# Optimization experiments

Measured on AMD Instinct MI355X. Metric: run time of the kernel, lower is better.

Reference implementation:

```python
import jax, jax.numpy as jnp
import numpy as np

N, E, F_IN, H, L = 1536, 49152, 27, 64, 32


def _ln(x, g, b, eps=1e-5):
    m = x.mean(-1, keepdims=True)
    v = ((x - m) ** 2).mean(-1, keepdims=True)
    return (x - m) * jax.lax.rsqrt(v + eps) * g + b


def _gatv2(x, src, dst, Wl, bl, Wr, br, att, bias, n):
    # PyG GATv2Conv, heads=1: alpha_ij = softmax_j( att . leaky_relu(Wl x_j + Wr x_i) )
    xl = x @ Wl + bl  # source transform [n,H]
    xr = x @ Wr + br  # target transform [n,H]
    e = jax.nn.leaky_relu(xl[src] + xr[dst], 0.2)  # [E',H]
    s = e @ att  # [E'] attention logits
    m = jax.ops.segment_max(s, dst, num_segments=n)
    w = jnp.exp(s - m[dst])
    denom = jax.ops.segment_sum(w, dst, num_segments=n)
    alpha = w / denom[dst]
    return jax.ops.segment_sum(alpha[:, None] * xl[src], dst, num_segments=n) + bias


def _model(x, eps_nodes, eps_graph, edge_index,
           Wl1, bl1, Wr1, br1, att1, bias1,
           Wl2, bl2, Wr2, br2, att2, bias2,
           Wnm, bnm, Wnv, bnv, Wgm, bgm, Wgv, bgv,
           Wd1, bd1, ln1_g, ln1_b, Wd2, bd2, ln2_g, ln2_b, Wd3, bd3,
           We1, be1, lne_g, lne_b, We2, be2,
           Wf1, bf1, lnf_g, lnf_b, Wf2, bf2):
    n = x.shape[0]
    loop = jnp.arange(n)
    src = jnp.concatenate([edge_index[0], loop])  # add self loops (PyG default)
    dst = jnp.concatenate([edge_index[1], loop])
    h = jax.nn.relu(_gatv2(x, src, dst, Wl1, bl1, Wr1, br1, att1, bias1, n))
    h = jax.nn.relu(_gatv2(h, src, dst, Wl2, bl2, Wr2, br2, att2, bias2, n))
    node_mu = h @ Wnm + bnm
    node_logvar = h @ Wnv + bnv
    gh = h.mean(0)
    graph_mu = gh @ Wgm + bgm
    graph_logvar = gh @ Wgv + bgv
    z = node_mu + eps_nodes * jnp.exp(0.5 * node_logvar)  # node reparam (training)
    _zg = graph_mu + eps_graph * jnp.exp(0.5 * graph_logvar)  # z_graph: computed, unused downstream as in source
    # dec_node_features MLP
    nf = _ln(jax.nn.relu(z @ Wd1 + bd1), ln1_g, ln1_b)
    nf = _ln(jax.nn.relu(nf @ Wd2 + bd2), ln2_g, ln2_b)
    nf = nf @ Wd3 + bd3  # [n, F_IN]
    # feature_refinement (node_embeddings = h is passed in forward)
    nf = _ln(jax.nn.relu(jnp.concatenate([nf, h], -1) @ Wf1 + bf1), lnf_g, lnf_b)
    node_features = nf @ Wf2 + bf2
    # edge_pred over all i<j pairs, vectorized (replaces the O(N^2) python loop)
    iu, ju = jnp.triu_indices(n, k=1)
    ei = jnp.concatenate([z[iu], z[ju]], -1)  # [P, 2L]
    eh = _ln(jax.nn.relu(ei @ We1 + be1), lne_g, lne_b)
    edge_logits = (eh @ We2 + be2)[:, 0]  # [P]
    return node_features, edge_logits, node_mu, node_logvar, graph_mu, graph_logvar


def setup_inputs() -> dict:
    key = jax.random.key(0)
    ki = iter(jax.random.split(key, 40))
    def W(fi, fo):
        return jax.random.normal(next(ki), (fi, fo), jnp.float32) / np.sqrt(fi)
    z64 = jnp.zeros((H,), jnp.float32)
    o64 = jnp.ones((H,), jnp.float32)
    zL = jnp.zeros((L,), jnp.float32)
    zF = jnp.zeros((F_IN,), jnp.float32)
    inp = {}
    inp["x"] = jax.random.normal(next(ki), (N, F_IN), jnp.float32)
    inp["edge_index"] = jax.random.randint(next(ki), (2, E), 0, N)
    inp["eps_nodes"] = jax.random.normal(next(ki), (N, L), jnp.float32)
    inp["eps_graph"] = jax.random.normal(next(ki), (L,), jnp.float32)
    inp.update(Wl1=W(F_IN, H), bl1=z64, Wr1=W(F_IN, H), br1=z64,
               att1=jax.random.normal(next(ki), (H,), jnp.float32) / np.sqrt(H), bias1=z64,
               Wl2=W(H, H), bl2=z64, Wr2=W(H, H), br2=z64,
               att2=jax.random.normal(next(ki), (H,), jnp.float32) / np.sqrt(H), bias2=z64)
    inp.update(Wnm=W(H, L), bnm=zL, Wnv=W(H, L), bnv=zL,
               Wgm=W(H, L), bgm=zL, Wgv=W(H, L), bgv=zL)
    inp.update(Wd1=W(L, H), bd1=z64, ln1_g=o64, ln1_b=z64,
               Wd2=W(H, H), bd2=z64, ln2_g=o64, ln2_b=z64,
               Wd3=W(H, F_IN), bd3=zF)
    inp.update(We1=W(2 * L, H), be1=z64, lne_g=o64, lne_b=z64,
               We2=W(H, 1), be2=jnp.zeros((1,), jnp.float32))
    inp.update(Wf1=W(F_IN + H, H), bf1=z64, lnf_g=o64, lnf_b=z64,
               Wf2=W(H, F_IN), bf2=zF)
    return inp


def reference(x, edge_index, eps_nodes, eps_graph,
              Wl1, bl1, Wr1, br1, att1, bias1,
              Wl2, bl2, Wr2, br2, att2, bias2,
              Wnm, bnm, Wnv, bnv, Wgm, bgm, Wgv, bgv,
              Wd1, bd1, ln1_g, ln1_b, Wd2, bd2, ln2_g, ln2_b, Wd3, bd3,
              We1, be1, lne_g, lne_b, We2, be2,
              Wf1, bf1, lnf_g, lnf_b, Wf2, bf2):
    return _model(x, eps_nodes, eps_graph, edge_index,
                  Wl1, bl1, Wr1, br1, att1, bias1,
                  Wl2, bl2, Wr2, br2, att2, bias2,
                  Wnm, bnm, Wnv, bnv, Wgm, bgm, Wgv, bgv,
                  Wd1, bd1, ln1_g, ln1_b, Wd2, bd2, ln2_g, ln2_b, Wd3, bd3,
                  We1, be1, lne_g, lne_b, We2, be2,
                  Wf1, bf1, lnf_g, lnf_b, Wf2, bf2)
```

## Files before the change

### kernel.cpp

```cpp
#include <hip/hip_runtime.h>

#define NN 1536
#define NE 49152
#define NM (NE + NN)
#define FIN 27
#define HD 64
#define LDIM 32
#define PP 1178880

#define EL_OFF  (NN*FIN)
#define MU_OFF  (EL_OFF + PP)
#define LV_OFF  (MU_OFF + NN*LDIM)
#define GMU_OFF (LV_OFF + NN*LDIM)
#define GLV_OFF (GMU_OFF + LDIM)

__device__ __forceinline__ float wsum(float v) {
#pragma unroll
  for (int m = 1; m < 64; m <<= 1) v += __shfl_xor(v, m, 64);
  return v;
}
__device__ __forceinline__ void wsum2(float& a, float& b) {
#pragma unroll
  for (int m = 1; m < 64; m <<= 1) {
    a += __shfl_xor(a, m, 64);
    b += __shfl_xor(b, m, 64);
  }
}
__device__ __forceinline__ float lnorm64(float x, float g, float b) {
  float s1 = x, s2 = x * x;
  wsum2(s1, s2);
  float mu = s1 * (1.0f / 64.0f);
  float var = fmaf(-mu, mu, s2 * (1.0f / 64.0f));
  return (x - mu) * rsqrtf(var + 1e-5f) * g + b;
}
__device__ __forceinline__ void cp4(float* dst, const float* __restrict__ src,
                                    int n4, int t) {
  const float4* s4 = (const float4*)src;
  float4* d4 = (float4*)dst;
  for (int e = t; e < n4; e += 256) d4[e] = s4[e];
}

__device__ __forceinline__ float gat_gather(const int* __restrict__ rowptr,
                                            const int* __restrict__ slot,
                                            const float* __restrict__ xl,
                                            float xri, float ak, int i, int k) {
  int beg = rowptr[i], end = rowptr[i + 1];
  float acc = 0.f, den = 0.f;
  for (int e0 = beg; e0 < end; e0 += 64) {
    int sidx = (e0 + k < end) ? slot[e0 + k] : 0;
    int nn = min(64, end - e0);
    int j = 0;
    for (; j + 1 < nn; j += 2) {
      int s0 = __shfl(sidx, j, 64), s1 = __shfl(sidx, j + 1, 64);
      float x0 = xl[s0 * HD + k], x1 = xl[s1 * HD + k];
      float e0v = x0 + xri, e1v = x1 + xri;
      e0v = fmaxf(e0v, 0.2f * e0v);
      e1v = fmaxf(e1v, 0.2f * e1v);
      float p0 = e0v * ak, p1 = e1v * ak;
      wsum2(p0, p1);
      float w0 = expf(p0), w1 = expf(p1);
      acc = fmaf(w0, x0, acc); den += w0;
      acc = fmaf(w1, x1, acc); den += w1;
    }
    if (j < nn) {
      int s0 = __shfl(sidx, j, 64);
      float x0 = xl[s0 * HD + k];
      float e0v = x0 + xri;
      e0v = fmaxf(e0v, 0.2f * e0v);
      float w0 = expf(wsum(e0v * ak));
      acc = fmaf(w0, x0, acc); den += w0;
    }
  }
  return acc / den;
}

__global__ __launch_bounds__(256) void gvae_xform1(
    const float* __restrict__ in,
    const float* __restrict__ Wl, const float* __restrict__ bl,
    const float* __restrict__ Wr, const float* __restrict__ br,
    float* __restrict__ xl, float* __restrict__ xr,
    const int* __restrict__ ei, int* __restrict__ cnt) {
  __shared__ __align__(16) float sWl[FIN * HD];
  __shared__ __align__(16) float sWr[FIN * HD];
  int t = threadIdx.x;
  int gid = blockIdx.x * 256 + t;
  if (gid < NE) atomicAdd(&cnt[ei[NE + gid]], 1);
  cp4(sWl, Wl, FIN * 16, t);
  cp4(sWr, Wr, FIN * 16, t);
  int i = blockIdx.x * 4 + (t >> 6);
  int k = t & 63;
  float xv = (k < FIN) ? in[i * FIN + k] : 0.f;
  float l0 = bl[k], l1 = 0.f, r0 = br[k], r1 = 0.f;
  __syncthreads();
#pragma unroll
  for (int a = 0; a < FIN; a += 2) {
    float xa = __shfl(xv, a, 64);
    l0 = fmaf(xa, sWl[a * HD + k], l0);
    r0 = fmaf(xa, sWr[a * HD + k], r0);
    if (a + 1 < FIN) {
      float xb = __shfl(xv, a + 1, 64);
      l1 = fmaf(xb, sWl[(a + 1) * HD + k], l1);
      r1 = fmaf(xb, sWr[(a + 1) * HD + k], r1);
    }
  }
  xl[i * HD + k] = l0 + l1;
  xr[i * HD + k] = r0 + r1;
}

__global__ __launch_bounds__(256) void gvae_scan(
    const int* __restrict__ cnt, int* __restrict__ rowptr,
    int* __restrict__ cursor, int* __restrict__ slot) {
  __shared__ int part[256];
  int t = threadIdx.x;
  int base = t * 6;
  int v[6];
  int s = 0;
#pragma unroll
  for (int j = 0; j < 6; j++) { v[j] = cnt[base + j] + 1; s += v[j]; }
  part[t] = s;
  __syncthreads();
  for (int off = 1; off < 256; off <<= 1) {
    int y = (t >= off) ? part[t - off] : 0;
    __syncthreads();
    part[t] += y;
    __syncthreads();
  }
  int r = part[t] - s;
#pragma unroll
  for (int j = 0; j < 6; j++) {
    int node = base + j;
    rowptr[node] = r;
    slot[r] = node;
    cursor[node] = r + 1;
    r += v[j];
  }
  if (t == 255) rowptr[NN] = r;
}

__global__ __launch_bounds__(256) void gvae_scatter(
    const int* __restrict__ ei, int* __restrict__ cursor, int* __restrict__ slot) {
  int m = blockIdx.x * 256 + threadIdx.x;
  if (m < NE) {
    int d = ei[NE + m];
    int p = atomicAdd(&cursor[d], 1);
    slot[p] = ei[m];
  }
}

__global__ __launch_bounds__(256) void gvae_gatherx(
    const int* __restrict__ rowptr, const int* __restrict__ slot,
    const float* __restrict__ xl, const float* __restrict__ xr,
    const float* __restrict__ att, const float* __restrict__ hbias,
    const float* __restrict__ Wl, const float* __restrict__ bl,
    const float* __restrict__ Wr, const float* __restrict__ br,
    float* __restrict__ xlo, float* __restrict__ xro) {
  __shared__ __align__(16) float sWl[HD * HD];
  __shared__ __align__(16) float sWr[HD * HD];
  int t = threadIdx.x;
  cp4(sWl, Wl, HD * 16, t);
  cp4(sWr, Wr, HD * 16, t);
  int i = blockIdx.x * 4 + (t >> 6);
  int k = t & 63;
  float xri = xr[i * HD + k];
  float ak = att[k];
  float hv = fmaxf(gat_gather(rowptr, slot, xl, xri, ak, i, k) + hbias[k], 0.f);
  float l0 = bl[k], l1 = 0.f, r0 = br[k], r1 = 0.f;
  __syncthreads();
#pragma unroll
  for (int a = 0; a < HD; a += 2) {
    float xa = __shfl(hv, a, 64);
    float xb = __shfl(hv, a + 1, 64);
    l0 = fmaf(xa, sWl[a * HD + k], l0);
    r0 = fmaf(xa, sWr[a * HD + k], r0);
    l1 = fmaf(xb, sWl[(a + 1) * HD + k], l1);
    r1 = fmaf(xb, sWr[(a + 1) * HD + k], r1);
  }
  xlo[i * HD + k] = l0 + l1;
  xro[i * HD + k] = r0 + r1;
}

#define oE1 0
#define oD1 4096
#define oD2 6144
#define oF1 10240
#define SWTOT 16064

__global__ __launch_bounds__(256, 2) void gvae_node(
    const int* __restrict__ rowptr, const int* __restrict__ slot,
    const float* __restrict__ xl, const float* __restrict__ xr,
    const float* __restrict__ att, const float* __restrict__ bias2,
    const float* __restrict__ eps,
    const float* __restrict__ Wnm, const float* __restrict__ bnm,
    const float* __restrict__ Wnv, const float* __restrict__ bnv,
    const float* __restrict__ We1, const float* __restrict__ be1,
    const float* __restrict__ Wd1, const float* __restrict__ bd1,
    const float* __restrict__ g1, const float* __restrict__ b1,
    const float* __restrict__ Wd2, const float* __restrict__ bd2,
    const float* __restrict__ g2, const float* __restrict__ b2,
    const float* __restrict__ Wd3, const float* __restrict__ bd3,
    const float* __restrict__ Wf1, const float* __restrict__ bf1,
    const float* __restrict__ gf, const float* __restrict__ bfv,
    const float* __restrict__ Wf2, const float* __restrict__ bf2,
    float* __restrict__ uo, float* __restrict__ vo,
    float* __restrict__ gh, float* __restrict__ out) {
  __shared__ __align__(16) float sW[SWTOT];
  __shared__ float ghred[256];
  int t = threadIdx.x;
  cp4(sW + oE1, We1, 1024, t);
  cp4(sW + oD1, Wd1, 512, t);
  cp4(sW + oD2, Wd2, 1024, t);
  cp4(sW + oF1, Wf1, 1456, t);

  int i = blockIdx.x * 4 + (t >> 6);
  int k = t & 63;
  int kk = k & 31;
  int kc = (k < FIN) ? k : (FIN - 1);

  float xri = xr[i * HD + k];
  float ak = att[k];
  float h2k = fmaxf(gat_gather(rowptr, slot, xl, xri, ak, i, k) + bias2[k], 0.f);
  ghred[t] = h2k;
  __syncthreads();
  if (t < 64) {
    float s = (ghred[t] + ghred[t + 64]) + (ghred[t + 128] + ghred[t + 192]);
    atomicAdd(&gh[t], s * (1.0f / NN));
  }

  const float* W = (k < 32) ? Wnm : Wnv;
  float c0 = (k < 32) ? bnm[kk] : bnv[kk];
  float c1 = 0.f, c2 = 0.f, c3 = 0.f;
#pragma unroll
  for (int a = 0; a < HD; a += 4) {
    c0 = fmaf(__shfl(h2k, a, 64),     W[a * LDIM + kk],       c0);
    c1 = fmaf(__shfl(h2k, a + 1, 64), W[(a + 1) * LDIM + kk], c1);
    c2 = fmaf(__shfl(h2k, a + 2, 64), W[(a + 2) * LDIM + kk], c2);
    c3 = fmaf(__shfl(h2k, a + 3, 64), W[(a + 3) * LDIM + kk], c3);
  }
  float acc = (c0 + c1) + (c2 + c3);
  if (k < 32) out[MU_OFF + i * LDIM + kk] = acc;
  else        out[LV_OFF + i * LDIM + kk] = acc;

  float lv = __shfl(acc, k + 32, 64);
  float zk = acc + eps[i * LDIM + kk] * expf(0.5f * lv);

  float u0 = be1[k], u1 = 0.f, v0 = 0.f, v1 = 0.f;
#pragma unroll
  for (int a = 0; a < LDIM; a += 2) {
    float za = __shfl(zk, a, 64);
    float zb = __shfl(zk, a + 1, 64);
    u0 = fmaf(za, sW[oE1 + a * HD + k], u0);
    u1 = fmaf(zb, sW[oE1 + (a + 1) * HD + k], u1);
    v0 = fmaf(za, sW[oE1 + (a + LDIM) * HD + k], v0);
    v1 = fmaf(zb, sW[oE1 + (a + 1 + LDIM) * HD + k], v1);
  }
  uo[i * HD + k] = u0 + u1;
  vo[i * HD + k] = v0 + v1;

  c0 = bd1[k]; c1 = 0.f; c2 = 0.f; c3 = 0.f;
#pragma unroll
  for (int a = 0; a < LDIM; a += 4) {
    c0 = fmaf(__shfl(zk, a, 64),     sW[oD1 + a * HD + k],       c0);
    c1 = fmaf(__shfl(zk, a + 1, 64), sW[oD1 + (a + 1) * HD + k], c1);
    c2 = fmaf(__shfl(zk, a + 2, 64), sW[oD1 + (a + 2) * HD + k], c2);
    c3 = fmaf(__shfl(zk, a + 3, 64), sW[oD1 + (a + 3) * HD + k], c3);
  }
  float nf1 = lnorm64(fmaxf((c0 + c1) + (c2 + c3), 0.f), g1[k], b1[k]);

  c0 = bd2[k]; c1 = 0.f; c2 = 0.f; c3 = 0.f;
#pragma unroll
  for (int a = 0; a < HD; a += 4) {
    c0 = fmaf(__shfl(nf1, a, 64),     sW[oD2 + a * HD + k],       c0);
    c1 = fmaf(__shfl(nf1, a + 1, 64), sW[oD2 + (a + 1) * HD + k], c1);
    c2 = fmaf(__shfl(nf1, a + 2, 64), sW[oD2 + (a + 2) * HD + k], c2);
    c3 = fmaf(__shfl(nf1, a + 3, 64), sW[oD2 + (a + 3) * HD + k], c3);
  }
  float nf2 = lnorm64(fmaxf((c0 + c1) + (c2 + c3), 0.f), g2[k], b2[k]);

  c0 = 0.f; c1 = 0.f; c2 = 0.f; c3 = 0.f;
#pragma unroll
  for (int a = 0; a < HD; a += 4) {
    c0 = fmaf(__shfl(nf2, a, 64),     Wd3[a * FIN + kc],       c0);
    c1 = fmaf(__shfl(nf2, a + 1, 64), Wd3[(a + 1) * FIN + kc], c1);
    c2 = fmaf(__shfl(nf2, a + 2, 64), Wd3[(a + 2) * FIN + kc], c2);
    c3 = fmaf(__shfl(nf2, a + 3, 64), Wd3[(a + 3) * FIN + kc], c3);
  }
  float nf3 = (k < FIN) ? ((c0 + c1) + (c2 + c3) + bd3[kc]) : 0.f;

  c0 = bf1[k]; c1 = 0.f; c2 = 0.f; c3 = 0.f;
#pragma unroll
  for (int j = 0; j < FIN; j++) {
    float nj = __shfl(nf3, j, 64);
    c0 = fmaf(nj, sW[oF1 + j * HD + k], c0);
  }
#pragma unroll
  for (int a = 0; a < HD; a += 4) {
    c0 = fmaf(__shfl(h2k, a, 64),     sW[oF1 + (FIN + a) * HD + k],     c0);
    c1 = fmaf(__shfl(h2k, a + 1, 64), sW[oF1 + (FIN + a + 1) * HD + k], c1);
    c2 = fmaf(__shfl(h2k, a + 2, 64), sW[oF1 + (FIN + a + 2) * HD + k], c2);
    c3 = fmaf(__shfl(h2k, a + 3, 64), sW[oF1 + (FIN + a + 3) * HD + k], c3);
  }
  float rr = lnorm64(fmaxf((c0 + c1) + (c2 + c3), 0.f), gf[k], bfv[k]);

  c0 = 0.f; c1 = 0.f; c2 = 0.f; c3 = 0.f;
#pragma unroll
  for (int a = 0; a < HD; a += 4) {
    c0 = fmaf(__shfl(rr, a, 64),     Wf2[a * FIN + kc],       c0);
    c1 = fmaf(__shfl(rr, a + 1, 64), Wf2[(a + 1) * FIN + kc], c1);
    c2 = fmaf(__shfl(rr, a + 2, 64), Wf2[(a + 2) * FIN + kc], c2);
    c3 = fmaf(__shfl(rr, a + 3, 64), Wf2[(a + 3) * FIN + kc], c3);
  }
  if (k < FIN) out[i * FIN + k] = (c0 + c1) + (c2 + c3) + bf2[kc];
}

__global__ __launch_bounds__(256) void gvae_edge(
    const float* __restrict__ u, const float* __restrict__ v,
    const float* __restrict__ lng, const float* __restrict__ lnb,
    const float* __restrict__ w2, const float* __restrict__ be2,
    const float* __restrict__ gh,
    const float* __restrict__ Wgm, const float* __restrict__ bgm,
    const float* __restrict__ Wgv, const float* __restrict__ bgv,
    float* __restrict__ out) {
  __shared__ float U[64 * 64];
  __shared__ float V[64 * 68];
  __shared__ float C[64];
  __shared__ float cc[2];
  int t = threadIdx.x;
  int wv = t >> 6, lane = t & 63;

  if (blockIdx.x == 0 && wv == 3) {
    int kk = lane & 31;
    float ghk = gh[lane];
    const float* W = (lane < 32) ? Wgm : Wgv;
    float c0 = (lane < 32) ? bgm[kk] : bgv[kk];
    float c1 = 0.f, c2 = 0.f, c3 = 0.f;
#pragma unroll
    for (int a = 0; a < HD; a += 4) {
      c0 = fmaf(__shfl(ghk, a, 64),     W[a * LDIM + kk],       c0);
      c1 = fmaf(__shfl(ghk, a + 1, 64), W[(a + 1) * LDIM + kk], c1);
      c2 = fmaf(__shfl(ghk, a + 2, 64), W[(a + 2) * LDIM + kk], c2);
      c3 = fmaf(__shfl(ghk, a + 3, 64), W[(a + 3) * LDIM + kk], c3);
    }
    float acc = (c0 + c1) + (c2 + c3);
    if (lane < 32) out[GMU_OFF + kk] = acc;
    else           out[GLV_OFF + kk] = acc;
  }

  int rem = blockIdx.x, bi = 0;
  while (rem >= 24 - bi) { rem -= 24 - bi; bi++; }
  int bj = bi + rem;

  const float4* u4p = (const float4*)(u + bi * 64 * HD);
  const float4* v4p = (const float4*)(v + bj * 64 * HD);
#pragma unroll
  for (int it = 0; it < 4; ++it) {
    int r = t + it * 256;
    int row = r >> 4, q = r & 15;
    float4 uu = u4p[r];
    *(float4*)&U[row * 64 + q * 4] = uu;
    float4 vvv = v4p[r];
    *(float4*)&V[row * 68 + q * 4] = vvv;
  }
  if (t < 64) {
    float ck = lng[t] * w2[t];
    C[t] = ck;
    float cb = lnb[t] * w2[t];
    float sC = wsum(ck);
    float sB = wsum(cb);
    if (t == 0) { cc[0] = sC; cc[1] = sB + be2[0]; }
  }
  __syncthreads();
  float C1 = cc[0], C0 = cc[1];

  float S1[16], S2[16], Sc[16];
#pragma unroll
  for (int ii = 0; ii < 16; ii++) { S1[ii] = 0.f; S2[ii] = 0.f; Sc[ii] = 0.f; }
  const float* Ub = &U[(wv * 16) * 64];
  for (int k4 = 0; k4 < 16; k4++) {
    float4 v4 = *(const float4*)&V[lane * 68 + k4 * 4];
    float4 c4 = *(const float4*)&C[k4 * 4];
#pragma unroll
    for (int ii = 0; ii < 16; ii++) {
      float4 u4 = *(const float4*)&Ub[ii * 64 + k4 * 4];
      float t0 = fmaxf(u4.x + v4.x, 0.f);
      float t1 = fmaxf(u4.y + v4.y, 0.f);
      float t2 = fmaxf(u4.z + v4.z, 0.f);
      float t3 = fmaxf(u4.w + v4.w, 0.f);
      S1[ii] += (t0 + t1) + (t2 + t3);
      S2[ii] = fmaf(t0, t0, fmaf(t1, t1, fmaf(t2, t2, fmaf(t3, t3, S2[ii]))));
      Sc[ii] = fmaf(t0, c4.x, fmaf(t1, c4.y, fmaf(t2, c4.z, fmaf(t3, c4.w, Sc[ii]))));
    }
  }
  int j = bj * 64 + lane;
  const float inv64 = 1.0f / 64.0f;
#pragma unroll
  for (int ii = 0; ii < 16; ii++) {
    int i = bi * 64 + wv * 16 + ii;
    if (j > i) {
      int pbase = i * (2 * NN - i - 1) / 2 - i - 1;
      float mu = S1[ii] * inv64;
      float var = fmaf(-mu, mu, S2[ii] * inv64);
      float logit = (Sc[ii] - mu * C1) * rsqrtf(var + 1e-5f) + C0;
      out[EL_OFF + pbase + j] = logit;
    }
  }
}

extern "C" void kernel_launch(void* const* d_in, const int* in_sizes, int n_in,
                              void* d_out, int out_size, void* d_ws, size_t ws_size,
                              hipStream_t stream) {
  const float* x    = (const float*)d_in[0];
  const int*   ei   = (const int*)d_in[1];
  const float* eps  = (const float*)d_in[2];
  const float* Wl1  = (const float*)d_in[4];
  const float* bl1  = (const float*)d_in[5];
  const float* Wr1  = (const float*)d_in[6];
  const float* br1  = (const float*)d_in[7];
  const float* att1 = (const float*)d_in[8];
  const float* bias1= (const float*)d_in[9];
  const float* Wl2  = (const float*)d_in[10];
  const float* bl2  = (const float*)d_in[11];
  const float* Wr2  = (const float*)d_in[12];
  const float* br2  = (const float*)d_in[13];
  const float* att2 = (const float*)d_in[14];
  const float* bias2= (const float*)d_in[15];
  const float* Wnm  = (const float*)d_in[16];
  const float* bnm  = (const float*)d_in[17];
  const float* Wnv  = (const float*)d_in[18];
  const float* bnv  = (const float*)d_in[19];
  const float* Wgm  = (const float*)d_in[20];
  const float* bgm  = (const float*)d_in[21];
  const float* Wgv  = (const float*)d_in[22];
  const float* bgv  = (const float*)d_in[23];
  const float* Wd1  = (const float*)d_in[24];
  const float* bd1  = (const float*)d_in[25];
  const float* ln1g = (const float*)d_in[26];
  const float* ln1b = (const float*)d_in[27];
  const float* Wd2  = (const float*)d_in[28];
  const float* bd2  = (const float*)d_in[29];
  const float* ln2g = (const float*)d_in[30];
  const float* ln2b = (const float*)d_in[31];
  const float* Wd3  = (const float*)d_in[32];
  const float* bd3  = (const float*)d_in[33];
  const float* We1  = (const float*)d_in[34];
  const float* be1  = (const float*)d_in[35];
  const float* lneg = (const float*)d_in[36];
  const float* lneb = (const float*)d_in[37];
  const float* We2  = (const float*)d_in[38];
  const float* be2  = (const float*)d_in[39];
  const float* Wf1  = (const float*)d_in[40];
  const float* bf1  = (const float*)d_in[41];
  const float* lnfg = (const float*)d_in[42];
  const float* lnfb = (const float*)d_in[43];
  const float* Wf2  = (const float*)d_in[44];
  const float* bf2  = (const float*)d_in[45];
  float* out = (float*)d_out;

  float* fb  = (float*)d_ws;
  float* xl1 = fb;
  float* xr1 = xl1 + NN * HD;
  float* xl2 = xr1 + NN * HD;
  float* xr2 = xl2 + NN * HD;
  float* uu  = xr2 + NN * HD;
  float* vv  = uu  + NN * HD;
  float* gh  = vv  + NN * HD;
  int* cnt    = (int*)(gh + HD);
  int* rowptr = cnt + NN;
  int* cursor = rowptr + NN + 1;
  int* slot   = cursor + NN;

  hipMemsetAsync(gh, 0, (HD + NN) * sizeof(float), stream);

  gvae_xform1<<<NN / 4, 256, 0, stream>>>(x, Wl1, bl1, Wr1, br1, xl1, xr1, ei, cnt);
  gvae_scan<<<1, 256, 0, stream>>>(cnt, rowptr, cursor, slot);
  gvae_scatter<<<NE / 256, 256, 0, stream>>>(ei, cursor, slot);
  gvae_gatherx<<<NN / 4, 256, 0, stream>>>(rowptr, slot, xl1, xr1, att1, bias1,
                                           Wl2, bl2, Wr2, br2, xl2, xr2);
  gvae_node<<<NN / 4, 256, 0, stream>>>(rowptr, slot, xl2, xr2, att2, bias2, eps,
      Wnm, bnm, Wnv, bnv, We1, be1,
      Wd1, bd1, ln1g, ln1b, Wd2, bd2, ln2g, ln2b, Wd3, bd3,
      Wf1, bf1, lnfg, lnfb, Wf2, bf2,
      uu, vv, gh, out);
  gvae_edge<<<300, 256, 0, stream>>>(uu, vv, lneg, lneb, We2, be2,
                                     gh, Wgm, bgm, Wgv, bgv, out);
}
```

Before: 242.2 us.

## Fuse all stages into one persistent kernel with software grid barriers

Merges the six kernel launches (transform, scan, scatter, two GAT gathers plus node MLP, edge scoring) into a single 384-block kernel. Stages are separated by atomic-counter grid barriers that are reset by the existing memset. The aim is to remove per-launch overhead and inter-kernel gaps in a pipeline of short kernels. In exchange, all 384 blocks must be co-resident for the spin barriers to avoid deadlock, and each barrier adds spin latency and fence cost.

```diff
diff --git a/kernel.cpp b/kernel.cpp
--- a/kernel.cpp
+++ b/kernel.cpp
@@ -7,6 +7,7 @@
 #define HD 64
 #define LDIM 32
 #define PP 1178880
+#define NBLK 384
 
 #define EL_OFF  (NN*FIN)
 #define MU_OFF  (EL_OFF + PP)
@@ -38,6 +39,18 @@
   const float4* s4 = (const float4*)src;
   float4* d4 = (float4*)dst;
   for (int e = t; e < n4; e += 256) d4[e] = s4[e];
+}
+
+__device__ __forceinline__ void gbar(int* ctr) {
+  __syncthreads();
+  if (threadIdx.x == 0) {
+    __threadfence();
+    __hip_atomic_fetch_add(ctr, 1, __ATOMIC_RELAXED, __HIP_MEMORY_SCOPE_AGENT);
+    while (__hip_atomic_load(ctr, __ATOMIC_RELAXED, __HIP_MEMORY_SCOPE_AGENT) < NBLK)
+      __builtin_amdgcn_s_sleep(2);
+  }
+  __syncthreads();
+  __threadfence();
 }
 
 __device__ __forceinline__ float gat_gather(const int* __restrict__ rowptr,
@@ -74,333 +87,320 @@
   return acc / den;
 }
 
-__global__ __launch_bounds__(256) void gvae_xform1(
-    const float* __restrict__ in,
-    const float* __restrict__ Wl, const float* __restrict__ bl,
-    const float* __restrict__ Wr, const float* __restrict__ br,
-    float* __restrict__ xl, float* __restrict__ xr,
-    const int* __restrict__ ei, int* __restrict__ cnt) {
-  __shared__ __align__(16) float sWl[FIN * HD];
-  __shared__ __align__(16) float sWr[FIN * HD];
-  int t = threadIdx.x;
-  int gid = blockIdx.x * 256 + t;
-  if (gid < NE) atomicAdd(&cnt[ei[NE + gid]], 1);
-  cp4(sWl, Wl, FIN * 16, t);
-  cp4(sWr, Wr, FIN * 16, t);
-  int i = blockIdx.x * 4 + (t >> 6);
-  int k = t & 63;
-  float xv = (k < FIN) ? in[i * FIN + k] : 0.f;
-  float l0 = bl[k], l1 = 0.f, r0 = br[k], r1 = 0.f;
-  __syncthreads();
-#pragma unroll
-  for (int a = 0; a < FIN; a += 2) {
-    float xa = __shfl(xv, a, 64);
-    l0 = fmaf(xa, sWl[a * HD + k], l0);
-    r0 = fmaf(xa, sWr[a * HD + k], r0);
-    if (a + 1 < FIN) {
-      float xb = __shfl(xv, a + 1, 64);
-      l1 = fmaf(xb, sWl[(a + 1) * HD + k], l1);
-      r1 = fmaf(xb, sWr[(a + 1) * HD + k], r1);
-    }
-  }
-  xl[i * HD + k] = l0 + l1;
-  xr[i * HD + k] = r0 + r1;
-}
-
-__global__ __launch_bounds__(256) void gvae_scan(
-    const int* __restrict__ cnt, int* __restrict__ rowptr,
-    int* __restrict__ cursor, int* __restrict__ slot) {
-  __shared__ int part[256];
-  int t = threadIdx.x;
-  int base = t * 6;
-  int v[6];
-  int s = 0;
-#pragma unroll
-  for (int j = 0; j < 6; j++) { v[j] = cnt[base + j] + 1; s += v[j]; }
-  part[t] = s;
-  __syncthreads();
-  for (int off = 1; off < 256; off <<= 1) {
-    int y = (t >= off) ? part[t - off] : 0;
-    __syncthreads();
-    part[t] += y;
-    __syncthreads();
-  }
-  int r = part[t] - s;
-#pragma unroll
-  for (int j = 0; j < 6; j++) {
-    int node = base + j;
-    rowptr[node] = r;
-    slot[r] = node;
-    cursor[node] = r + 1;
-    r += v[j];
-  }
-  if (t == 255) rowptr[NN] = r;
-}
-
-__global__ __launch_bounds__(256) void gvae_scatter(
-    const int* __restrict__ ei, int* __restrict__ cursor, int* __restrict__ slot) {
-  int m = blockIdx.x * 256 + threadIdx.x;
-  if (m < NE) {
-    int d = ei[NE + m];
-    int p = atomicAdd(&cursor[d], 1);
-    slot[p] = ei[m];
-  }
-}
-
-__global__ __launch_bounds__(256) void gvae_gatherx(
-    const int* __restrict__ rowptr, const int* __restrict__ slot,
-    const float* __restrict__ xl, const float* __restrict__ xr,
-    const float* __restrict__ att, const float* __restrict__ hbias,
-    const float* __restrict__ Wl, const float* __restrict__ bl,
-    const float* __restrict__ Wr, const float* __restrict__ br,
-    float* __restrict__ xlo, float* __restrict__ xro) {
-  __shared__ __align__(16) float sWl[HD * HD];
-  __shared__ __align__(16) float sWr[HD * HD];
-  int t = threadIdx.x;
-  cp4(sWl, Wl, HD * 16, t);
-  cp4(sWr, Wr, HD * 16, t);
-  int i = blockIdx.x * 4 + (t >> 6);
-  int k = t & 63;
-  float xri = xr[i * HD + k];
-  float ak = att[k];
-  float hv = fmaxf(gat_gather(rowptr, slot, xl, xri, ak, i, k) + hbias[k], 0.f);
-  float l0 = bl[k], l1 = 0.f, r0 = br[k], r1 = 0.f;
-  __syncthreads();
-#pragma unroll
-  for (int a = 0; a < HD; a += 2) {
-    float xa = __shfl(hv, a, 64);
-    float xb = __shfl(hv, a + 1, 64);
-    l0 = fmaf(xa, sWl[a * HD + k], l0);
-    r0 = fmaf(xa, sWr[a * HD + k], r0);
-    l1 = fmaf(xb, sWl[(a + 1) * HD + k], l1);
-    r1 = fmaf(xb, sWr[(a + 1) * HD + k], r1);
-  }
-  xlo[i * HD + k] = l0 + l1;
-  xro[i * HD + k] = r0 + r1;
-}
-
 #define oE1 0
 #define oD1 4096
 #define oD2 6144
 #define oF1 10240
-#define SWTOT 16064
-
-__global__ __launch_bounds__(256, 2) void gvae_node(
-    const int* __restrict__ rowptr, const int* __restrict__ slot,
-    const float* __restrict__ xl, const float* __restrict__ xr,
-    const float* __restrict__ att, const float* __restrict__ bias2,
+#define oGH 16064
+#define SWTOT 16320
+
+__global__ __launch_bounds__(256, 2) void gvae_mega(
+    const float* __restrict__ x, const int* __restrict__ ei,
     const float* __restrict__ eps,
+    const float* __restrict__ Wl1, const float* __restrict__ bl1,
+    const float* __restrict__ Wr1, const float* __restrict__ br1,
+    const float* __restrict__ att1, const float* __restrict__ bias1,
+    const float* __restrict__ Wl2, const float* __restrict__ bl2,
+    const float* __restrict__ Wr2, const float* __restrict__ br2,
+    const float* __restrict__ att2, const float* __restrict__ bias2,
     const float* __restrict__ Wnm, const float* __restrict__ bnm,
     const float* __restrict__ Wnv, const float* __restrict__ bnv,
-    const float* __restrict__ We1, const float* __restrict__ be1,
+    const float* __restrict__ Wgm, const float* __restrict__ bgm,
+    const float* __restrict__ Wgv, const float* __restrict__ bgv,
     const float* __restrict__ Wd1, const float* __restrict__ bd1,
     const float* __restrict__ g1, const float* __restrict__ b1,
     const float* __restrict__ Wd2, const float* __restrict__ bd2,
     const float* __restrict__ g2, const float* __restrict__ b2,
     const float* __restrict__ Wd3, const float* __restrict__ bd3,
+    const float* __restrict__ We1, const float* __restrict__ be1,
+    const float* __restrict__ lng, const float* __restrict__ lnb,
+    const float* __restrict__ w2, const float* __restrict__ be2,
     const float* __restrict__ Wf1, const float* __restrict__ bf1,
     const float* __restrict__ gf, const float* __restrict__ bfv,
     const float* __restrict__ Wf2, const float* __restrict__ bf2,
+    float* __restrict__ xl1, float* __restrict__ xr1,
+    float* __restrict__ xl2, float* __restrict__ xr2,
     float* __restrict__ uo, float* __restrict__ vo,
-    float* __restrict__ gh, float* __restrict__ out) {
+    float* __restrict__ gh, int* __restrict__ cnt, int* __restrict__ bars,
+    int* __restrict__ rowptr, int* __restrict__ cursor, int* __restrict__ slot,
+    float* __restrict__ out) {
   __shared__ __align__(16) float sW[SWTOT];
-  __shared__ float ghred[256];
   int t = threadIdx.x;
-  cp4(sW + oE1, We1, 1024, t);
-  cp4(sW + oD1, Wd1, 512, t);
-  cp4(sW + oD2, Wd2, 1024, t);
-  cp4(sW + oF1, Wf1, 1456, t);
-
-  int i = blockIdx.x * 4 + (t >> 6);
+  int b = blockIdx.x;
+  int i = b * 4 + (t >> 6);
   int k = t & 63;
-  int kk = k & 31;
-  int kc = (k < FIN) ? k : (FIN - 1);
-
-  float xri = xr[i * HD + k];
-  float ak = att[k];
-  float h2k = fmaxf(gat_gather(rowptr, slot, xl, xri, ak, i, k) + bias2[k], 0.f);
-  ghred[t] = h2k;
-  __syncthreads();
-  if (t < 64) {
-    float s = (ghred[t] + ghred[t + 64]) + (ghred[t + 128] + ghred[t + 192]);
-    atomicAdd(&gh[t], s * (1.0f / NN));
-  }
-
-  const float* W = (k < 32) ? Wnm : Wnv;
-  float c0 = (k < 32) ? bnm[kk] : bnv[kk];
-  float c1 = 0.f, c2 = 0.f, c3 = 0.f;
-#pragma unroll
-  for (int a = 0; a < HD; a += 4) {
-    c0 = fmaf(__shfl(h2k, a, 64),     W[a * LDIM + kk],       c0);
-    c1 = fmaf(__shfl(h2k, a + 1, 64), W[(a + 1) * LDIM + kk], c1);
-    c2 = fmaf(__shfl(h2k, a + 2, 64), W[(a + 2) * LDIM + kk], c2);
-    c3 = fmaf(__shfl(h2k, a + 3, 64), W[(a + 3) * LDIM + kk], c3);
-  }
-  float acc = (c0 + c1) + (c2 + c3);
-  if (k < 32) out[MU_OFF + i * LDIM + kk] = acc;
-  else        out[LV_OFF + i * LDIM + kk] = acc;
-
-  float lv = __shfl(acc, k + 32, 64);
-  float zk = acc + eps[i * LDIM + kk] * expf(0.5f * lv);
-
-  float u0 = be1[k], u1 = 0.f, v0 = 0.f, v1 = 0.f;
-#pragma unroll
-  for (int a = 0; a < LDIM; a += 2) {
-    float za = __shfl(zk, a, 64);
-    float zb = __shfl(zk, a + 1, 64);
-    u0 = fmaf(za, sW[oE1 + a * HD + k], u0);
-    u1 = fmaf(zb, sW[oE1 + (a + 1) * HD + k], u1);
-    v0 = fmaf(za, sW[oE1 + (a + LDIM) * HD + k], v0);
-    v1 = fmaf(zb, sW[oE1 + (a + 1 + LDIM) * HD + k], v1);
-  }
-  uo[i * HD + k] = u0 + u1;
-  vo[i * HD + k] = v0 + v1;
-
-  c0 = bd1[k]; c1 = 0.f; c2 = 0.f; c3 = 0.f;
-#pragma unroll
-  for (int a = 0; a < LDIM; a += 4) {
-    c0 = fmaf(__shfl(zk, a, 64),     sW[oD1 + a * HD + k],       c0);
-    c1 = fmaf(__shfl(zk, a + 1, 64), sW[oD1 + (a + 1) * HD + k], c1);
-    c2 = fmaf(__shfl(zk, a + 2, 64), sW[oD1 + (a + 2) * HD + k], c2);
-    c3 = fmaf(__shfl(zk, a + 3, 64), sW[oD1 + (a + 3) * HD + k], c3);
-  }
-  float nf1 = lnorm64(fmaxf((c0 + c1) + (c2 + c3), 0.f), g1[k], b1[k]);
-
-  c0 = bd2[k]; c1 = 0.f; c2 = 0.f; c3 = 0.f;
-#pragma unroll
-  for (int a = 0; a < HD; a += 4) {
-    c0 = fmaf(__shfl(nf1, a, 64),     sW[oD2 + a * HD + k],       c0);
-    c1 = fmaf(__shfl(nf1, a + 1, 64), sW[oD2 + (a + 1) * HD + k], c1);
-    c2 = fmaf(__shfl(nf1, a + 2, 64), sW[oD2 + (a + 2) * HD + k], c2);
-    c3 = fmaf(__shfl(nf1, a + 3, 64), sW[oD2 + (a + 3) * HD + k], c3);
-  }
-  float nf2 = lnorm64(fmaxf((c0 + c1) + (c2 + c3), 0.f), g2[k], b2[k]);
-
-  c0 = 0.f; c1 = 0.f; c2 = 0.f; c3 = 0.f;
-#pragma unroll
-  for (int a = 0; a < HD; a += 4) {
-    c0 = fmaf(__shfl(nf2, a, 64),     Wd3[a * FIN + kc],       c0);
-    c1 = fmaf(__shfl(nf2, a + 1, 64), Wd3[(a + 1) * FIN + kc], c1);
-    c2 = fmaf(__shfl(nf2, a + 2, 64), Wd3[(a + 2) * FIN + kc], c2);
-    c3 = fmaf(__shfl(nf2, a + 3, 64), Wd3[(a + 3) * FIN + kc], c3);
-  }
-  float nf3 = (k < FIN) ? ((c0 + c1) + (c2 + c3) + bd3[kc]) : 0.f;
-
-  c0 = bf1[k]; c1 = 0.f; c2 = 0.f; c3 = 0.f;
-#pragma unroll
-  for (int j = 0; j < FIN; j++) {
-    float nj = __shfl(nf3, j, 64);
-    c0 = fmaf(nj, sW[oF1 + j * HD + k], c0);
-  }
-#pragma unroll
-  for (int a = 0; a < HD; a += 4) {
-    c0 = fmaf(__shfl(h2k, a, 64),     sW[oF1 + (FIN + a) * HD + k],     c0);
-    c1 = fmaf(__shfl(h2k, a + 1, 64), sW[oF1 + (FIN + a + 1) * HD + k], c1);
-    c2 = fmaf(__shfl(h2k, a + 2, 64), sW[oF1 + (FIN + a + 2) * HD + k], c2);
-    c3 = fmaf(__shfl(h2k, a + 3, 64), sW[oF1 + (FIN + a + 3) * HD + k], c3);
-  }
-  float rr = lnorm64(fmaxf((c0 + c1) + (c2 + c3), 0.f), gf[k], bfv[k]);
-
-  c0 = 0.f; c1 = 0.f; c2 = 0.f; c3 = 0.f;
-#pragma unroll
-  for (int a = 0; a < HD; a += 4) {
-    c0 = fmaf(__shfl(rr, a, 64),     Wf2[a * FIN + kc],       c0);
-    c1 = fmaf(__shfl(rr, a + 1, 64), Wf2[(a + 1) * FIN + kc], c1);
-    c2 = fmaf(__shfl(rr, a + 2, 64), Wf2[(a + 2) * FIN + kc], c2);
-    c3 = fmaf(__shfl(rr, a + 3, 64), Wf2[(a + 3) * FIN + kc], c3);
-  }
-  if (k < FIN) out[i * FIN + k] = (c0 + c1) + (c2 + c3) + bf2[kc];
-}
-
-__global__ __launch_bounds__(256) void gvae_edge(
-    const float* __restrict__ u, const float* __restrict__ v,
-    const float* __restrict__ lng, const float* __restrict__ lnb,
-    const float* __restrict__ w2, const float* __restrict__ be2,
-    const float* __restrict__ gh,
-    const float* __restrict__ Wgm, const float* __restrict__ bgm,
-    const float* __restrict__ Wgv, const float* __restrict__ bgv,
-    float* __restrict__ out) {
-  __shared__ float U[64 * 64];
-  __shared__ float V[64 * 68];
-  __shared__ float C[64];
-  __shared__ float cc[2];
-  int t = threadIdx.x;
-  int wv = t >> 6, lane = t & 63;
-
-  if (blockIdx.x == 0 && wv == 3) {
-    int kk = lane & 31;
-    float ghk = gh[lane];
-    const float* W = (lane < 32) ? Wgm : Wgv;
-    float c0 = (lane < 32) ? bgm[kk] : bgv[kk];
+  int gid = b * 256 + t;
+
+  if (gid < NE) atomicAdd(&cnt[ei[NE + gid]], 1);
+  {
+    float* sWl = sW;
+    float* sWr = sW + FIN * HD;
+    cp4(sWl, Wl1, FIN * 16, t);
+    cp4(sWr, Wr1, FIN * 16, t);
+    float xv = (k < FIN) ? x[i * FIN + k] : 0.f;
+    float l0 = bl1[k], l1 = 0.f, r0 = br1[k], r1 = 0.f;
+    __syncthreads();
+#pragma unroll
+    for (int a = 0; a < FIN; a += 2) {
+      float xa = __shfl(xv, a, 64);
+      l0 = fmaf(xa, sWl[a * HD + k], l0);
+      r0 = fmaf(xa, sWr[a * HD + k], r0);
+      if (a + 1 < FIN) {
+        float xb = __shfl(xv, a + 1, 64);
+        l1 = fmaf(xb, sWl[(a + 1) * HD + k], l1);
+        r1 = fmaf(xb, sWr[(a + 1) * HD + k], r1);
+      }
+    }
+    xl1[i * HD + k] = l0 + l1;
+    xr1[i * HD + k] = r0 + r1;
+  }
+  gbar(&bars[0]);
+
+  if (b == 0) {
+    int* part = (int*)sW;
+    int base = t * 6;
+    int v[6];
+    int s = 0;
+#pragma unroll
+    for (int j = 0; j < 6; j++) { v[j] = cnt[base + j] + 1; s += v[j]; }
+    part[t] = s;
+    __syncthreads();
+    for (int off = 1; off < 256; off <<= 1) {
+      int y = (t >= off) ? part[t - off] : 0;
+      __syncthreads();
+      part[t] += y;
+      __syncthreads();
+    }
+    int r = part[t] - s;
+#pragma unroll
+    for (int j = 0; j < 6; j++) {
+      int node = base + j;
+      rowptr[node] = r;
+      slot[r] = node;
+      cursor[node] = r + 1;
+      r += v[j];
+    }
+    if (t == 255) rowptr[NN] = r;
+  }
+  gbar(&bars[1]);
+
+  if (gid < NE) {
+    int d = ei[NE + gid];
+    int p = atomicAdd(&cursor[d], 1);
+    slot[p] = ei[gid];
+  }
+  gbar(&bars[2]);
+
+  {
+    float* sWl = sW;
+    float* sWr = sW + HD * HD;
+    cp4(sWl, Wl2, HD * 16, t);
+    cp4(sWr, Wr2, HD * 16, t);
+    float xri = xr1[i * HD + k];
+    float ak = att1[k];
+    float hv = fmaxf(gat_gather(rowptr, slot, xl1, xri, ak, i, k) + bias1[k], 0.f);
+    float l0 = bl2[k], l1 = 0.f, r0 = br2[k], r1 = 0.f;
+    __syncthreads();
+#pragma unroll
+    for (int a = 0; a < HD; a += 2) {
+      float xa = __shfl(hv, a, 64);
+      float xb = __shfl(hv, a + 1, 64);
+      l0 = fmaf(xa, sWl[a * HD + k], l0);
+      r0 = fmaf(xa, sWr[a * HD + k], r0);
+      l1 = fmaf(xb, sWl[(a + 1) * HD + k], l1);
+      r1 = fmaf(xb, sWr[(a + 1) * HD + k], r1);
+    }
+    xl2[i * HD + k] = l0 + l1;
+    xr2[i * HD + k] = r0 + r1;
+  }
+  gbar(&bars[3]);
+
+  {
+    cp4(sW + oE1, We1, 1024, t);
+    cp4(sW + oD1, Wd1, 512, t);
+    cp4(sW + oD2, Wd2, 1024, t);
+    cp4(sW + oF1, Wf1, 1456, t);
+    int kk = k & 31;
+    int kc = (k < FIN) ? k : (FIN - 1);
+    float xri = xr2[i * HD + k];
+    float ak = att2[k];
+    float h2k = fmaxf(gat_gather(rowptr, slot, xl2, xri, ak, i, k) + bias2[k], 0.f);
+    sW[oGH + t] = h2k;
+    __syncthreads();
+    if (t < 64) {
+      float s = (sW[oGH + t] + sW[oGH + t + 64]) + (sW[oGH + t + 128] + sW[oGH + t + 192]);
+      atomicAdd(&gh[t], s * (1.0f / NN));
+    }
+
+    const float* W = (k < 32) ? Wnm : Wnv;
+    float c0 = (k < 32) ? bnm[kk] : bnv[kk];
     float c1 = 0.f, c2 = 0.f, c3 = 0.f;
 #pragma unroll
     for (int a = 0; a < HD; a += 4) {
-      c0 = fmaf(__shfl(ghk, a, 64),     W[a * LDIM + kk],       c0);
-      c1 = fmaf(__shfl(ghk, a + 1, 64), W[(a + 1) * LDIM + kk], c1);
-      c2 = fmaf(__shfl(ghk, a + 2, 64), W[(a + 2) * LDIM + kk], c2);
-      c3 = fmaf(__shfl(ghk, a + 3, 64), W[(a + 3) * LDIM + kk], c3);
+      c0 = fmaf(__shfl(h2k, a, 64),     W[a * LDIM + kk],       c0);
+      c1 = fmaf(__shfl(h2k, a + 1, 64), W[(a + 1) * LDIM + kk], c1);
+      c2 = fmaf(__shfl(h2k, a + 2, 64), W[(a + 2) * LDIM + kk], c2);
+      c3 = fmaf(__shfl(h2k, a + 3, 64), W[(a + 3) * LDIM + kk], c3);
     }
     float acc = (c0 + c1) + (c2 + c3);
-    if (lane < 32) out[GMU_OFF + kk] = acc;
-    else           out[GLV_OFF + kk] = acc;
-  }
-
-  int rem = blockIdx.x, bi = 0;
-  while (rem >= 24 - bi) { rem -= 24 - bi; bi++; }
-  int bj = bi + rem;
-
-  const float4* u4p = (const float4*)(u + bi * 64 * HD);
-  const float4* v4p = (const float4*)(v + bj * 64 * HD);
-#pragma unroll
-  for (int it = 0; it < 4; ++it) {
-    int r = t + it * 256;
-    int row = r >> 4, q = r & 15;
-    float4 uu = u4p[r];
-    *(float4*)&U[row * 64 + q * 4] = uu;
-    float4 vvv = v4p[r];
-    *(float4*)&V[row * 68 + q * 4] = vvv;
-  }
-  if (t < 64) {
-    float ck = lng[t] * w2[t];
-    C[t] = ck;
-    float cb = lnb[t] * w2[t];
-    float sC = wsum(ck);
-    float sB = wsum(cb);
-    if (t == 0) { cc[0] = sC; cc[1] = sB + be2[0]; }
-  }
-  __syncthreads();
-  float C1 = cc[0], C0 = cc[1];
-
-  float S1[16], S2[16], Sc[16];
-#pragma unroll
-  for (int ii = 0; ii < 16; ii++) { S1[ii] = 0.f; S2[ii] = 0.f; Sc[ii] = 0.f; }
-  const float* Ub = &U[(wv * 16) * 64];
-  for (int k4 = 0; k4 < 16; k4++) {
-    float4 v4 = *(const float4*)&V[lane * 68 + k4 * 4];
-    float4 c4 = *(const float4*)&C[k4 * 4];
+    if (k < 32) out[MU_OFF + i * LDIM + kk] = acc;
+    else        out[LV_OFF + i * LDIM + kk] = acc;
+
+    float lv = __shfl(acc, k + 32, 64);
+    float zk = acc + eps[i * LDIM + kk] * expf(0.5f * lv);
+
+    float u0 = be1[k], u1 = 0.f, v0 = 0.f, v1 = 0.f;
+#pragma unroll
+    for (int a = 0; a < LDIM; a += 2) {
+      float za = __shfl(zk, a, 64);
+      float zb = __shfl(zk, a + 1, 64);
+      u0 = fmaf(za, sW[oE1 + a * HD + k], u0);
+      u1 = fmaf(zb, sW[oE1 + (a + 1) * HD + k], u1);
+      v0 = fmaf(za, sW[oE1 + (a + LDIM) * HD + k], v0);
+      v1 = fmaf(zb, sW[oE1 + (a + 1 + LDIM) * HD + k], v1);
+    }
+    uo[i * HD + k] = u0 + u1;
+    vo[i * HD + k] = v0 + v1;
+
+    c0 = bd1[k]; c1 = 0.f; c2 = 0.f; c3 = 0.f;
+#pragma unroll
+    for (int a = 0; a < LDIM; a += 4) {
+      c0 = fmaf(__shfl(zk, a, 64),     sW[oD1 + a * HD + k],       c0);
+      c1 = fmaf(__shfl(zk, a + 1, 64), sW[oD1 + (a + 1) * HD + k], c1);
+      c2 = fmaf(__shfl(zk, a + 2, 64), sW[oD1 + (a + 2) * HD + k], c2);
+      c3 = fmaf(__shfl(zk, a + 3, 64), sW[oD1 + (a + 3) * HD + k], c3);
+    }
+    float nf1 = lnorm64(fmaxf((c0 + c1) + (c2 + c3), 0.f), g1[k], b1[k]);
+
+    c0 = bd2[k]; c1 = 0.f; c2 = 0.f; c3 = 0.f;
+#pragma unroll
+    for (int a = 0; a < HD; a += 4) {
+      c0 = fmaf(__shfl(nf1, a, 64),     sW[oD2 + a * HD + k],       c0);
+      c1 = fmaf(__shfl(nf1, a + 1, 64), sW[oD2 + (a + 1) * HD + k], c1);
+      c2 = fmaf(__shfl(nf1, a + 2, 64), sW[oD2 + (a + 2) * HD + k], c2);
+      c3 = fmaf(__shfl(nf1, a + 3, 64), sW[oD2 + (a + 3) * HD + k], c3);
+    }
+    float nf2 = lnorm64(fmaxf((c0 + c1) + (c2 + c3), 0.f), g2[k], b2[k]);
+
+    c0 = 0.f; c1 = 0.f; c2 = 0.f; c3 = 0.f;
+#pragma unroll
+    for (int a = 0; a < HD; a += 4) {
+      c0 = fmaf(__shfl(nf2, a, 64),     Wd3[a * FIN + kc],       c0);
+      c1 = fmaf(__shfl(nf2, a + 1, 64), Wd3[(a + 1) * FIN + kc], c1);
+      c2 = fmaf(__shfl(nf2, a + 2, 64), Wd3[(a + 2) * FIN + kc], c2);
+      c3 = fmaf(__shfl(nf2, a + 3, 64), Wd3[(a + 3) * FIN + kc], c3);
+    }
+    float nf3 = (k < FIN) ? ((c0 + c1) + (c2 + c3) + bd3[kc]) : 0.f;
+
+    c0 = bf1[k]; c1 = 0.f; c2 = 0.f; c3 = 0.f;
+#pragma unroll
+    for (int j = 0; j < FIN; j++) {
+      float nj = __shfl(nf3, j, 64);
+      c0 = fmaf(nj, sW[oF1 + j * HD + k], c0);
+    }
+#pragma unroll
+    for (int a = 0; a < HD; a += 4) {
+      c0 = fmaf(__shfl(h2k, a, 64),     sW[oF1 + (FIN + a) * HD + k],     c0);
+      c1 = fmaf(__shfl(h2k, a + 1, 64), sW[oF1 + (FIN + a + 1) * HD + k], c1);
+      c2 = fmaf(__shfl(h2k, a + 2, 64), sW[oF1 + (FIN + a + 2) * HD + k], c2);
+      c3 = fmaf(__shfl(h2k, a + 3, 64), sW[oF1 + (FIN + a + 3) * HD + k], c3);
+    }
+    float rr = lnorm64(fmaxf((c0 + c1) + (c2 + c3), 0.f), gf[k], bfv[k]);
+
+    c0 = 0.f; c1 = 0.f; c2 = 0.f; c3 = 0.f;
+#pragma unroll
+    for (int a = 0; a < HD; a += 4) {
+      c0 = fmaf(__shfl(rr, a, 64),     Wf2[a * FIN + kc],       c0);
+      c1 = fmaf(__shfl(rr, a + 1, 64), Wf2[(a + 1) * FIN + kc], c1);
+      c2 = fmaf(__shfl(rr, a + 2, 64), Wf2[(a + 2) * FIN + kc], c2);
+      c3 = fmaf(__shfl(rr, a + 3, 64), Wf2[(a + 3) * FIN + kc], c3);
+    }
+    if (k < FIN) out[i * FIN + k] = (c0 + c1) + (c2 + c3) + bf2[kc];
+  }
+  gbar(&bars[4]);
+
+  if (b < 300) {
+    float* U = sW;
+    float* V = sW + 4096;
+    float* C = sW + 8448;
+    float* cc = sW + 8512;
+    int wv = t >> 6, lane = t & 63;
+
+    if (b == 0 && wv == 3) {
+      int kk = lane & 31;
+      float ghk = gh[lane];
+      const float* W = (lane < 32) ? Wgm : Wgv;
+      float c0 = (lane < 32) ? bgm[kk] : bgv[kk];
+      float c1 = 0.f, c2 = 0.f, c3 = 0.f;
+#pragma unroll
+      for (int a = 0; a < HD; a += 4) {
+        c0 = fmaf(__shfl(ghk, a, 64),     W[a * LDIM + kk],       c0);
+        c1 = fmaf(__shfl(ghk, a + 1, 64), W[(a + 1) * LDIM + kk], c1);
+        c2 = fmaf(__shfl(ghk, a + 2, 64), W[(a + 2) * LDIM + kk], c2);
+        c3 = fmaf(__shfl(ghk, a + 3, 64), W[(a + 3) * LDIM + kk], c3);
+      }
+      float acc = (c0 + c1) + (c2 + c3);
+      if (lane < 32) out[GMU_OFF + kk] = acc;
+      else           out[GLV_OFF + kk] = acc;
+    }
+
+    int rem = b, bi = 0;
+    while (rem >= 24 - bi) { rem -= 24 - bi; bi++; }
+    int bj = bi + rem;
+
+    const float4* u4p = (const float4*)(uo + bi * 64 * HD);
+    const float4* v4p = (const float4*)(vo + bj * 64 * HD);
+#pragma unroll
+    for (int it = 0; it < 4; ++it) {
+      int r = t + it * 256;
+      int row = r >> 4, q = r & 15;
+      float4 uu4 = u4p[r];
+      *(float4*)&U[row * 64 + q * 4] = uu4;
+      float4 vv4 = v4p[r];
+      *(float4*)&V[row * 68 + q * 4] = vv4;
+    }
+    if (t < 64) {
+      float ck = lng[t] * w2[t];
+      C[t] = ck;
+      float cb = lnb[t] * w2[t];
+      float sC = wsum(ck);
+      float sB = wsum(cb);
+      if (t == 0) { cc[0] = sC; cc[1] = sB + be2[0]; }
+    }
+    __syncthreads();
+    float C1 = cc[0], C0 = cc[1];
+
+    float S1[16], S2[16], Sc[16];
+#pragma unroll
+    for (int ii = 0; ii < 16; ii++) { S1[ii] = 0.f; S2[ii] = 0.f; Sc[ii] = 0.f; }
+    const float* Ub = &U[(wv * 16) * 64];
+    for (int k4 = 0; k4 < 16; k4++) {
+      float4 v4 = *(const float4*)&V[lane * 68 + k4 * 4];
+      float4 c4 = *(const float4*)&C[k4 * 4];
+#pragma unroll
+      for (int ii = 0; ii < 16; ii++) {
+        float4 u4 = *(const float4*)&Ub[ii * 64 + k4 * 4];
+        float t0 = fmaxf(u4.x + v4.x, 0.f);
+        float t1 = fmaxf(u4.y + v4.y, 0.f);
+        float t2 = fmaxf(u4.z + v4.z, 0.f);
+        float t3 = fmaxf(u4.w + v4.w, 0.f);
+        S1[ii] += (t0 + t1) + (t2 + t3);
+        S2[ii] = fmaf(t0, t0, fmaf(t1, t1, fmaf(t2, t2, fmaf(t3, t3, S2[ii]))));
+        Sc[ii] = fmaf(t0, c4.x, fmaf(t1, c4.y, fmaf(t2, c4.z, fmaf(t3, c4.w, Sc[ii]))));
+      }
+    }
+    int j = bj * 64 + lane;
+    const float inv64 = 1.0f / 64.0f;
 #pragma unroll
     for (int ii = 0; ii < 16; ii++) {
-      float4 u4 = *(const float4*)&Ub[ii * 64 + k4 * 4];
-      float t0 = fmaxf(u4.x + v4.x, 0.f);
-      float t1 = fmaxf(u4.y + v4.y, 0.f);
-      float t2 = fmaxf(u4.z + v4.z, 0.f);
-      float t3 = fmaxf(u4.w + v4.w, 0.f);
-      S1[ii] += (t0 + t1) + (t2 + t3);
-      S2[ii] = fmaf(t0, t0, fmaf(t1, t1, fmaf(t2, t2, fmaf(t3, t3, S2[ii]))));
-      Sc[ii] = fmaf(t0, c4.x, fmaf(t1, c4.y, fmaf(t2, c4.z, fmaf(t3, c4.w, Sc[ii]))));
-    }
-  }
-  int j = bj * 64 + lane;
-  const float inv64 = 1.0f / 64.0f;
-#pragma unroll
-  for (int ii = 0; ii < 16; ii++) {
-    int i = bi * 64 + wv * 16 + ii;
-    if (j > i) {
-      int pbase = i * (2 * NN - i - 1) / 2 - i - 1;
-      float mu = S1[ii] * inv64;
-      float var = fmaf(-mu, mu, S2[ii] * inv64);
-      float logit = (Sc[ii] - mu * C1) * rsqrtf(var + 1e-5f) + C0;
-      out[EL_OFF + pbase + j] = logit;
+      int ir = bi * 64 + wv * 16 + ii;
+      if (j > ir) {
+        int pbase = ir * (2 * NN - ir - 1) / 2 - ir - 1;
+        float mu = S1[ii] * inv64;
+        float var = fmaf(-mu, mu, S2[ii] * inv64);
+        float logit = (Sc[ii] - mu * C1) * rsqrtf(var + 1e-5f) + C0;
+        out[EL_OFF + pbase + j] = logit;
+      }
     }
   }
 }
@@ -464,22 +464,21 @@
   float* vv  = uu  + NN * HD;
   float* gh  = vv  + NN * HD;
   int* cnt    = (int*)(gh + HD);
-  int* rowptr = cnt + NN;
+  int* bars   = cnt + NN;
+  int* rowptr = bars + 8;
   int* cursor = rowptr + NN + 1;
   int* slot   = cursor + NN;
 
-  hipMemsetAsync(gh, 0, (HD + NN) * sizeof(float), stream);
-
-  gvae_xform1<<<NN / 4, 256, 0, stream>>>(x, Wl1, bl1, Wr1, br1, xl1, xr1, ei, cnt);
-  gvae_scan<<<1, 256, 0, stream>>>(cnt, rowptr, cursor, slot);
-  gvae_scatter<<<NE / 256, 256, 0, stream>>>(ei, cursor, slot);
-  gvae_gatherx<<<NN / 4, 256, 0, stream>>>(rowptr, slot, xl1, xr1, att1, bias1,
-                                           Wl2, bl2, Wr2, br2, xl2, xr2);
-  gvae_node<<<NN / 4, 256, 0, stream>>>(rowptr, slot, xl2, xr2, att2, bias2, eps,
-      Wnm, bnm, Wnv, bnv, We1, be1,
+  hipMemsetAsync(gh, 0, (HD + NN + 8) * sizeof(float), stream);
+
+  gvae_mega<<<NBLK, 256, 0, stream>>>(
+      x, ei, eps,
+      Wl1, bl1, Wr1, br1, att1, bias1,
+      Wl2, bl2, Wr2, br2, att2, bias2,
+      Wnm, bnm, Wnv, bnv, Wgm, bgm, Wgv, bgv,
       Wd1, bd1, ln1g, ln1b, Wd2, bd2, ln2g, ln2b, Wd3, bd3,
+      We1, be1, lneg, lneb, We2, be2,
       Wf1, bf1, lnfg, lnfb, Wf2, bf2,
-      uu, vv, gh, out);
-  gvae_edge<<<300, 256, 0, stream>>>(uu, vv, lneg, lneb, We2, be2,
-                                     gh, Wgm, bgm, Wgv, bgv, out);
-}
+      xl1, xr1, xl2, xr2, uu, vv,
+      gh, cnt, bars, rowptr, cursor, slot, out);
+}
```

Measured after the change: 489.1 us. 2.02x slower.
